# Performance work log

Measured on AMD Instinct MI355X. Metric: run time of the kernel, lower is better.

The kernel has to match this reference:

```python
import jax, jax.numpy as jnp
import numpy as np

B, L, D, H = 2, 2048, 1024, 16
Dh = D // H

def setup_inputs() -> dict:
    key = jax.random.key(0)
    kx, kq, kk, kv, ko = jax.random.split(key, 5)
    scale = 1.0 / np.sqrt(D)
    return {
        "x": jax.random.normal(kx, (B, L, D), dtype=jnp.float32),
        "Wq": jax.random.normal(kq, (D, H, Dh), dtype=jnp.float32) * scale,
        "Wk": jax.random.normal(kk, (D, H, Dh), dtype=jnp.float32) * scale,
        "Wv": jax.random.normal(kv, (D, H, Dh), dtype=jnp.float32) * scale,
        "Wout": jax.random.normal(ko, (H, Dh, D), dtype=jnp.float32) * (1.0 / np.sqrt(D)),
    }

def reference(x, Wq, Wk, Wv, Wout):
    # QKV projections: [B,L,D] x [D,H,Dh] -> [B,L,H,Dh]
    q = jnp.einsum('bld,dhe->blhe', x, Wq)
    k = jnp.einsum('bld,dhe->blhe', x, Wk)
    v = jnp.einsum('bld,dhe->blhe', x, Wv)
    # scores [B,H,L,L]
    a = jnp.einsum('bqhd,bkhd->bhqk', q, k) / (Dh ** 0.5)
    Lq = x.shape[1]
    mask = jnp.tril(jnp.ones((1, 1, Lq, Lq), dtype=jnp.bool_))
    NEG_INF = jnp.finfo(jnp.float32).min
    a = jnp.where(mask, a, NEG_INF)
    a = jax.nn.softmax(a, axis=-1)
    o = jnp.einsum('bhqk,bkhd->bqhd', a, v)
    # output projection: [B,L,H,Dh] x [H,Dh,D] -> [B,L,D]
    return jnp.einsum('blhe,hed->bld', o, Wout)
```

## Files before the change

kernel.cpp:

```cpp
#include <hip/hip_runtime.h>

typedef __bf16 bf16x8 __attribute__((ext_vector_type(8)));
typedef __bf16 bf16x4 __attribute__((ext_vector_type(4)));
typedef float  floatx4 __attribute__((ext_vector_type(4)));
typedef float  floatx16 __attribute__((ext_vector_type(16)));

constexpr int Bc = 2, Lc = 2048, Dc = 1024, Hc = 16, Dhc = 64;
constexpr int Mr = 4096;

__device__ __forceinline__ void gl_lds16(const void* g, void* l) {
  __builtin_amdgcn_global_load_lds(
      (const __attribute__((address_space(1))) void*)g,
      (__attribute__((address_space(3))) void*)l, 16, 0, 0);
}

__global__ __launch_bounds__(256) void k_pack(const float* __restrict__ X,
                                              const float* __restrict__ W0,
                                              const float* __restrict__ W1,
                                              const float* __restrict__ W2,
                                              const float* __restrict__ W3,
                                              __bf16* __restrict__ Pw,
                                              __bf16* __restrict__ Px) {
  __shared__ __align__(16) __bf16 tile[64][66];
  int bid = blockIdx.x;
  int t = threadIdx.x;
  if (bid < 1024) {
    int z = bid >> 8, rem = bid & 255;
    int k0 = (rem & 15) << 6, n0 = (rem >> 4) << 6;
    const float* W = (z == 0) ? W0 : (z == 1) ? W1 : (z == 2) ? W2 : W3;
    __bf16* P = Pw + (size_t)z * 1024 * 1024;
    int r = t >> 2, cc = t & 3;
    const float4* src = (const float4*)&W[(size_t)(k0 + r) * 1024 + n0 + cc * 16];
#pragma unroll
    for (int i = 0; i < 4; i++) {
      float4 v = src[i];
      tile[r][cc * 16 + i * 4 + 0] = (__bf16)v.x;
      tile[r][cc * 16 + i * 4 + 1] = (__bf16)v.y;
      tile[r][cc * 16 + i * 4 + 2] = (__bf16)v.z;
      tile[r][cc * 16 + i * 4 + 3] = (__bf16)v.w;
    }
    __syncthreads();
#pragma unroll
    for (int i = 0; i < 2; i++) {
      int c = t + i * 256;
      int pl = c >> 6, nl = c & 63;
      bf16x8 o;
#pragma unroll
      for (int j = 0; j < 8; j++) o[j] = tile[pl * 8 + j][nl];
      *(bf16x8*)&P[((size_t)(k0 / 8 + pl) * 1024 + n0 + nl) * 8] = o;
    }
  } else {
    int xid = bid - 1024;
    int m0 = (xid & 63) << 6, p0 = (xid >> 6) << 2;
    int r = t >> 2, cc = t & 3;
    const float4* src = (const float4*)&X[(size_t)(m0 + r) * 1024 + p0 * 8 + cc * 8];
    float4 v0 = src[0], v1 = src[1];
    bf16x8 o;
    o[0] = (__bf16)v0.x; o[1] = (__bf16)v0.y; o[2] = (__bf16)v0.z; o[3] = (__bf16)v0.w;
    o[4] = (__bf16)v1.x; o[5] = (__bf16)v1.y; o[6] = (__bf16)v1.z; o[7] = (__bf16)v1.w;
    *(bf16x8*)&tile[0][r * 32 + cc * 8] = o;
    __syncthreads();
    int pc = t >> 6, ml = t & 63;
    bf16x8 q = *(bf16x8*)&tile[0][ml * 32 + pc * 8];
    *(bf16x8*)&Px[((size_t)(p0 + pc) * Mr + m0 + ml) * 8] = q;
  }
}

__global__ __launch_bounds__(256) void k_gemm_qkv(const __bf16* __restrict__ Ap8,
                                                  const __bf16* __restrict__ Bp8,
                                                  __bf16* __restrict__ Qb,
                                                  __bf16* __restrict__ Kb,
                                                  __bf16* __restrict__ Vb) {
  constexpr int K = 1024;
  constexpr int KCB = 2080;
  __shared__ __align__(16) char smem[4 * KCB * 4];
  char* As_raw = smem;
  char* Bs_raw = smem + 4 * KCB;
  int t = threadIdx.x, lane = t & 63, w = t >> 6;
  int lh = lane >> 5, l32 = lane & 31;
  int m0 = blockIdx.x * 128;
  int mat = blockIdx.y >> 3;
  const __bf16* Bbase = Bp8 + (size_t)mat * 1024 * 1024;
  int n0loc = (blockIdx.y & 7) * 128;
  int wm = (w & 1) * 64, wn = (w >> 1) * 64;
  floatx16 acc[2][2] = {};

  for (int k0 = 0; k0 < K; k0 += 32) {
    int kp = k0 >> 3;
    const __bf16* ga = Ap8 + ((size_t)(kp + w) * Mr + m0 + lane) * 8;
    const __bf16* gb = Bbase + ((size_t)(kp + w) * 1024 + n0loc + lane) * 8;
    char* la = As_raw + w * KCB;
    char* lb = Bs_raw + w * KCB;
    __syncthreads();
    gl_lds16(ga, la);
    gl_lds16(ga + 512, la + 1024);
    gl_lds16(gb, lb);
    gl_lds16(gb + 512, lb + 1024);
    __syncthreads();
    bf16x8 af[2][2], bfv[2][2];
#pragma unroll
    for (int s = 0; s < 2; s++) {
#pragma unroll
      for (int mt = 0; mt < 2; mt++)
        af[s][mt] = *(const bf16x8*)(As_raw + (2 * s + lh) * KCB + (wm + mt * 32 + l32) * 16);
#pragma unroll
      for (int nt = 0; nt < 2; nt++)
        bfv[s][nt] = *(const bf16x8*)(Bs_raw + (2 * s + lh) * KCB + (wn + nt * 32 + l32) * 16);
    }
#pragma unroll
    for (int s = 0; s < 2; s++)
#pragma unroll
      for (int mt = 0; mt < 2; mt++)
#pragma unroll
        for (int nt = 0; nt < 2; nt++)
          acc[mt][nt] = __builtin_amdgcn_mfma_f32_32x32x16_bf16(af[s][mt], bfv[s][nt], acc[mt][nt], 0, 0, 0);
  }

  __syncthreads();

  __bf16* sl = (__bf16*)(smem + w * (4 * KCB));
  int b = (m0 + wm) >> 11;
  int lbase = (m0 + wm) & 2047;
  int h = (n0loc + wn) >> 6;
  int bh2 = b * 16 + h;
  __bf16* dst;
  float scl = 1.0f;
  if (mat == 0) {
    dst = Qb + (((size_t)(bh2 * 64 + (lbase >> 5)) * 4) << 9);
    scl = 0.18033688011112042f;
  } else if (mat == 1) {
    dst = Kb + (((size_t)(bh2 * 32 + (lbase >> 6)) * 8) << 9);
  } else {
    dst = Vb + (((size_t)(bh2 * 32 + (lbase >> 6)) * 8) << 9);
  }
#pragma unroll
  for (int mt = 0; mt < 2; mt++)
#pragma unroll
    for (int nt = 0; nt < 2; nt++)
#pragma unroll
      for (int reg = 0; reg < 16; reg++) {
        int l_loc = mt * 32 + (reg & 3) + ((reg >> 2) << 3) + (lh << 2);
        int e = nt * 32 + l32;
        int off;
        if (mat == 0)
          off = ((l_loc >> 5) * 4 + ((l_loc >> 4) & 1) * 2 + (e >> 5)) * 512 +
                (((e >> 3) & 3) * 16 + (l_loc & 15)) * 8 + (e & 7);
        else if (mat == 1)
          off = ((l_loc >> 4) * 2 + (e >> 5)) * 512 +
                (((e >> 3) & 3) * 16 + (l_loc & 15)) * 8 + (e & 7);
        else
          off = ((e >> 4) * 2 + (l_loc >> 5)) * 512 +
                (((l_loc >> 2) & 3) * 16 + (e & 15)) * 8 + ((l_loc >> 4) & 1) * 4 + (l_loc & 3);
        sl[off] = (__bf16)(acc[mt][nt][reg] * scl);
      }
  __builtin_amdgcn_s_waitcnt(0);
#pragma unroll
  for (int i = 0; i < 8; i++) {
    int c = i * 64 + lane;
    bf16x8 v = *(bf16x8*)(sl + c * 8);
    *(bf16x8*)(dst + c * 8) = v;
  }
}

__global__ __launch_bounds__(256) void k_gemm_out(const __bf16* __restrict__ Ap8,
                                                  const __bf16* __restrict__ Bp8,
                                                  float* __restrict__ outF) {
  constexpr int K = 1024;
  constexpr int KCB_A = 2080;
  constexpr int KCB_B = 1056;
  __shared__ __align__(16) char smem[33792];
  char* As_raw = smem;
  char* Bs_raw = smem + 4 * KCB_A;
  int t = threadIdx.x, lane = t & 63, w = t >> 6;
  int lh = lane >> 5, l32 = lane & 31;
  int m0 = blockIdx.x * 128, n0 = blockIdx.y * 64;
  int wm = w * 32;
  floatx16 acc[2] = {};

  for (int k0 = 0; k0 < K; k0 += 32) {
    int kp = k0 >> 3;
    const __bf16* ga = Ap8 + ((size_t)(kp + w) * Mr + m0 + lane) * 8;
    const __bf16* gb = Bp8 + ((size_t)(kp + w) * 1024 + n0 + lane) * 8;
    char* la = As_raw + w * KCB_A;
    char* lb = Bs_raw + w * KCB_B;
    __syncthreads();
    gl_lds16(ga, la);
    gl_lds16(ga + 512, la + 1024);
    gl_lds16(gb, lb);
    __syncthreads();
    bf16x8 af[2], bfv[2][2];
#pragma unroll
    for (int s = 0; s < 2; s++) {
      af[s] = *(const bf16x8*)(As_raw + (2 * s + lh) * KCB_A + (wm + l32) * 16);
#pragma unroll
      for (int nt = 0; nt < 2; nt++)
        bfv[s][nt] = *(const bf16x8*)(Bs_raw + (2 * s + lh) * KCB_B + (nt * 32 + l32) * 16);
    }
#pragma unroll
    for (int s = 0; s < 2; s++)
#pragma unroll
      for (int nt = 0; nt < 2; nt++)
        acc[nt] = __builtin_amdgcn_mfma_f32_32x32x16_bf16(af[s], bfv[s][nt], acc[nt], 0, 0, 0);
  }

  __syncthreads();
  float* slf = (float*)(smem + w * 8448);
#pragma unroll
  for (int nt = 0; nt < 2; nt++)
#pragma unroll
    for (int reg = 0; reg < 16; reg++) {
      int rrow = (reg & 3) + ((reg >> 2) << 3) + (lh << 2);
      slf[rrow * 66 + nt * 32 + l32] = acc[nt][reg];
    }
  __builtin_amdgcn_s_waitcnt(0);
#pragma unroll
  for (int i = 0; i < 8; i++) {
    int c = i * 64 + lane;
    int row = c >> 4, sub = c & 15;
    float4 v = *(float4*)(slf + row * 66 + sub * 4);
    *(float4*)&outF[(size_t)(m0 + wm + row) * 1024 + n0 + sub * 4] = v;
  }
}

__global__ __launch_bounds__(256) void k_attn(const __bf16* __restrict__ Qf,
                                              const __bf16* __restrict__ Kf,
                                              const __bf16* __restrict__ Vf,
                                              __bf16* __restrict__ Op8) {
  __shared__ __align__(16) __bf16 POt[4][32][72];
  __shared__ float Pl[4][2][16];
  int t = threadIdx.x;
  int lane = t & 63, w = t >> 6;
  int quad = lane >> 4, l16 = lane & 15;
  int bid = blockIdx.x;
  int xcd = bid & 7, g = bid >> 3;
  int bh = xcd * 4 + (g & 3);
  int qt = 63 - (g >> 2);
  int qbase = qt * 32;

  const __bf16* Qp = Qf + (((size_t)(bh * 64 + qt) * 4) << 9) + lane * 8;
  bf16x8 qf[2][2];
#pragma unroll
  for (int mi = 0; mi < 2; mi++)
#pragma unroll
    for (int kk = 0; kk < 2; kk++)
      qf[mi][kk] = *(const bf16x8*)(Qp + ((mi * 2 + kk) << 9));

  floatx4 ot[4][2] = {};
  float l_s[2] = {0.f, 0.f};

  auto do_tile = [&](int kt, bool domask) {
    int kbase = kt * 64;
    const __bf16* Kp = Kf + (((size_t)(bh * 32 + kt) * 8) << 9) + lane * 8;
    const __bf16* Vp = Vf + (((size_t)(bh * 32 + kt) * 8) << 9) + lane * 8;
    bf16x8 ka[4][2], va[4][2];
#pragma unroll
    for (int kb = 0; kb < 4; kb++)
#pragma unroll
      for (int kk = 0; kk < 2; kk++) {
        ka[kb][kk] = *(const bf16x8*)(Kp + ((kb * 2 + kk) << 9));
        va[kb][kk] = *(const bf16x8*)(Vp + ((kb * 2 + kk) << 9));
      }

    floatx4 st[4][2] = {};
#pragma unroll
    for (int kb = 0; kb < 4; kb++)
#pragma unroll
      for (int mi = 0; mi < 2; mi++) {
        st[kb][mi] = __builtin_amdgcn_mfma_f32_16x16x32_bf16(ka[kb][0], qf[mi][0], st[kb][mi], 0, 0, 0);
        st[kb][mi] = __builtin_amdgcn_mfma_f32_16x16x32_bf16(ka[kb][1], qf[mi][1], st[kb][mi], 0, 0, 0);
      }

    bf16x8 pb[2][2];
#pragma unroll
    for (int mi = 0; mi < 2; mi++) {
      int q_g = qbase + mi * 16 + l16;
      float pv[4][4];
      float psum = 0.f;
#pragma unroll
      for (int kb = 0; kb < 4; kb++)
#pragma unroll
        for (int r = 0; r < 4; r++) {
          float v = st[kb][mi][r];
          if (domask) {
            int key = kbase + kb * 16 + quad * 4 + r;
            if (key > q_g) v = -__builtin_inff();
          }
          float p = __builtin_amdgcn_exp2f(v);
          pv[kb][r] = p;
          psum += p;
        }
      l_s[mi] += psum;
#pragma unroll
      for (int kp = 0; kp < 2; kp++) {
        bf16x8 p8;
#pragma unroll
        for (int j = 0; j < 4; j++) {
          p8[j] = (__bf16)pv[kp * 2][j];
          p8[j + 4] = (__bf16)pv[kp * 2 + 1][j];
        }
        pb[mi][kp] = p8;
      }
    }

#pragma unroll
    for (int kbd = 0; kbd < 4; kbd++)
#pragma unroll
      for (int mi = 0; mi < 2; mi++) {
        ot[kbd][mi] = __builtin_amdgcn_mfma_f32_16x16x32_bf16(va[kbd][0], pb[mi][0], ot[kbd][mi], 0, 0, 0);
        ot[kbd][mi] = __builtin_amdgcn_mfma_f32_16x16x32_bf16(va[kbd][1], pb[mi][1], ot[kbd][mi], 0, 0, 0);
      }
  };

  int nkt = ((qt * 32 + 31) >> 6) + 1;
  for (int kt = w; kt < nkt - 1; kt += 4) do_tile(kt, false);
  if (((nkt - 1) & 3) == w) do_tile(nkt - 1, true);

#pragma unroll
  for (int mi = 0; mi < 2; mi++) {
    l_s[mi] += __shfl_xor(l_s[mi], 16);
    l_s[mi] += __shfl_xor(l_s[mi], 32);
  }

#pragma unroll
  for (int mi = 0; mi < 2; mi++) {
    if (quad == 0) Pl[w][mi][l16] = l_s[mi];
#pragma unroll
    for (int kbd = 0; kbd < 4; kbd++) {
      bf16x4 p4;
#pragma unroll
      for (int r = 0; r < 4; r++) p4[r] = (__bf16)ot[kbd][mi][r];
      *(bf16x4*)&POt[w][mi * 16 + l16][kbd * 16 + quad * 4] = p4;
    }
  }
  __syncthreads();

  int oct = lane >> 3, rl = lane & 7;
  int ql = w * 8 + rl;
  float lstar = 0.f;
#pragma unroll
  for (int ww = 0; ww < 4; ww++) lstar += Pl[ww][ql >> 4][ql & 15];
  float inv = 1.f / lstar;
  float accv[8] = {};
#pragma unroll
  for (int ww = 0; ww < 4; ww++) {
    bf16x8 pv8 = *(const bf16x8*)&POt[ww][ql][oct * 8];
#pragma unroll
    for (int j = 0; j < 8; j++) accv[j] += (float)pv8[j];
  }
  bf16x8 ov;
#pragma unroll
  for (int j = 0; j < 8; j++) ov[j] = (__bf16)(accv[j] * inv);
  int b = bh >> 4, h = bh & 15;
  size_t row = (size_t)b * Lc + qbase + ql;
  *(bf16x8*)&Op8[((size_t)(h * 8 + oct) * Mr + row) * 8] = ov;
}

extern "C" void kernel_launch(void* const* d_in, const int* in_sizes, int n_in,
                              void* d_out, int out_size, void* d_ws, size_t ws_size,
                              hipStream_t stream) {
  const float* x  = (const float*)d_in[0];
  const float* Wq = (const float*)d_in[1];
  const float* Wk = (const float*)d_in[2];
  const float* Wv = (const float*)d_in[3];
  const float* Wo = (const float*)d_in[4];
  float* out = (float*)d_out;

  if (ws_size < (size_t)50331648) return;
  __bf16* xb   = (__bf16*)d_ws;
  __bf16* wqkv = xb + (size_t)Mr * Dc;
  __bf16* wot  = wqkv + (size_t)3 * Dc * Dc;
  __bf16* Qfr  = wot + (size_t)Dc * Dc;
  __bf16* Kfr  = Qfr + (size_t)Mr * Dc;
  __bf16* Vfr  = Kfr + (size_t)Mr * Dc;
  __bf16* Op8  = Vfr + (size_t)Mr * Dc;

  k_pack<<<3072, 256, 0, stream>>>(x, Wq, Wk, Wv, Wo, wqkv, xb);

  k_gemm_qkv<<<dim3(32, 24), 256, 0, stream>>>(xb, wqkv, Qfr, Kfr, Vfr);

  k_attn<<<dim3(2048), 256, 0, stream>>>(Qfr, Kfr, Vfr, Op8);

  k_gemm_out<<<dim3(32, 16), 256, 0, stream>>>(Op8, wot, out);
}
```

Measured before the change: 162.1 us.

## Double-buffer LDS tiles in QKV and output projection GEMMs

Both projection GEMM kernels now split shared memory into two stage buffers. The next K-tile's global-to-LDS DMA loads are issued right after the barrier, while MFMAs run on the current buffer, which removes one barrier per iteration and hides load latency. The shared memory footprint is unchanged. Overlap depends on the compiler not inserting a conservative vmcnt wait before the LDS reads of the current buffer.

```diff
diff --git a/kernel.cpp b/kernel.cpp
--- a/kernel.cpp
+++ b/kernel.cpp
@@ -71,11 +71,9 @@
                                                   __bf16* __restrict__ Qb,
                                                   __bf16* __restrict__ Kb,
                                                   __bf16* __restrict__ Vb) {
-  constexpr int K = 1024;
   constexpr int KCB = 2080;
-  __shared__ __align__(16) char smem[4 * KCB * 4];
-  char* As_raw = smem;
-  char* Bs_raw = smem + 4 * KCB;
+  constexpr int HB = 4 * KCB;
+  __shared__ __align__(16) char smem[4 * HB];
   int t = threadIdx.x, lane = t & 63, w = t >> 6;
   int lh = lane >> 5, l32 = lane & 31;
   int m0 = blockIdx.x * 128;
@@ -85,27 +83,33 @@
   int wm = (w & 1) * 64, wn = (w >> 1) * 64;
   floatx16 acc[2][2] = {};
 
-  for (int k0 = 0; k0 < K; k0 += 32) {
-    int kp = k0 >> 3;
+  auto issue = [&](int it, char* buf) {
+    int kp = it << 2;
     const __bf16* ga = Ap8 + ((size_t)(kp + w) * Mr + m0 + lane) * 8;
     const __bf16* gb = Bbase + ((size_t)(kp + w) * 1024 + n0loc + lane) * 8;
-    char* la = As_raw + w * KCB;
-    char* lb = Bs_raw + w * KCB;
-    __syncthreads();
+    char* la = buf + w * KCB;
+    char* lb = buf + HB + w * KCB;
     gl_lds16(ga, la);
     gl_lds16(ga + 512, la + 1024);
     gl_lds16(gb, lb);
     gl_lds16(gb + 512, lb + 1024);
+  };
+
+  issue(0, smem);
+  for (int it = 0; it < 32; it++) {
+    char* cur = smem + (it & 1) * (2 * HB);
+    char* nxt = smem + ((it & 1) ^ 1) * (2 * HB);
     __syncthreads();
+    if (it < 31) issue(it + 1, nxt);
     bf16x8 af[2][2], bfv[2][2];
 #pragma unroll
     for (int s = 0; s < 2; s++) {
 #pragma unroll
       for (int mt = 0; mt < 2; mt++)
-        af[s][mt] = *(const bf16x8*)(As_raw + (2 * s + lh) * KCB + (wm + mt * 32 + l32) * 16);
+        af[s][mt] = *(const bf16x8*)(cur + (2 * s + lh) * KCB + (wm + mt * 32 + l32) * 16);
 #pragma unroll
       for (int nt = 0; nt < 2; nt++)
-        bfv[s][nt] = *(const bf16x8*)(Bs_raw + (2 * s + lh) * KCB + (wn + nt * 32 + l32) * 16);
+        bfv[s][nt] = *(const bf16x8*)(cur + HB + (2 * s + lh) * KCB + (wn + nt * 32 + l32) * 16);
     }
 #pragma unroll
     for (int s = 0; s < 2; s++)
@@ -118,7 +122,7 @@
 
   __syncthreads();
 
-  __bf16* sl = (__bf16*)(smem + w * (4 * KCB));
+  __bf16* sl = (__bf16*)(smem + w * HB);
   int b = (m0 + wm) >> 11;
   int lbase = (m0 + wm) & 2047;
   int h = (n0loc + wn) >> 6;
@@ -165,36 +169,40 @@
 __global__ __launch_bounds__(256) void k_gemm_out(const __bf16* __restrict__ Ap8,
                                                   const __bf16* __restrict__ Bp8,
                                                   float* __restrict__ outF) {
-  constexpr int K = 1024;
   constexpr int KCB_A = 2080;
   constexpr int KCB_B = 1056;
+  constexpr int BUF = 4 * KCB_A + 4 * KCB_B;
   __shared__ __align__(16) char smem[33792];
-  char* As_raw = smem;
-  char* Bs_raw = smem + 4 * KCB_A;
   int t = threadIdx.x, lane = t & 63, w = t >> 6;
   int lh = lane >> 5, l32 = lane & 31;
   int m0 = blockIdx.x * 128, n0 = blockIdx.y * 64;
   int wm = w * 32;
   floatx16 acc[2] = {};
 
-  for (int k0 = 0; k0 < K; k0 += 32) {
-    int kp = k0 >> 3;
+  auto issue = [&](int it, char* buf) {
+    int kp = it << 2;
     const __bf16* ga = Ap8 + ((size_t)(kp + w) * Mr + m0 + lane) * 8;
     const __bf16* gb = Bp8 + ((size_t)(kp + w) * 1024 + n0 + lane) * 8;
-    char* la = As_raw + w * KCB_A;
-    char* lb = Bs_raw + w * KCB_B;
-    __syncthreads();
+    char* la = buf + w * KCB_A;
+    char* lb = buf + 4 * KCB_A + w * KCB_B;
     gl_lds16(ga, la);
     gl_lds16(ga + 512, la + 1024);
     gl_lds16(gb, lb);
+  };
+
+  issue(0, smem);
+  for (int it = 0; it < 32; it++) {
+    char* cur = smem + (it & 1) * BUF;
+    char* nxt = smem + ((it & 1) ^ 1) * BUF;
     __syncthreads();
+    if (it < 31) issue(it + 1, nxt);
     bf16x8 af[2], bfv[2][2];
 #pragma unroll
     for (int s = 0; s < 2; s++) {
-      af[s] = *(const bf16x8*)(As_raw + (2 * s + lh) * KCB_A + (wm + l32) * 16);
+      af[s] = *(const bf16x8*)(cur + (2 * s + lh) * KCB_A + (wm + l32) * 16);
 #pragma unroll
       for (int nt = 0; nt < 2; nt++)
-        bfv[s][nt] = *(const bf16x8*)(Bs_raw + (2 * s + lh) * KCB_B + (nt * 32 + l32) * 16);
+        bfv[s][nt] = *(const bf16x8*)(cur + 4 * KCB_A + (2 * s + lh) * KCB_B + (nt * 32 + l32) * 16);
     }
 #pragma unroll
     for (int s = 0; s < 2; s++)
```

Measured after the change: 158.7 us. 2.1% less time.
